# Kernel optimization log

Hardware: AMD Instinct MI355X
Metric: run time of the kernel (lower is better)

## Reference

```python
import jax, jax.numpy as jnp
import numpy as np

N, D, H1, K = 4096, 128, 256, 128


def setup_inputs() -> dict:
    key = jax.random.key(0)
    ks = jax.random.split(key, 8)
    A = jax.random.uniform(ks[3], (D, D), dtype=jnp.float32)
    A = A * (1.0 - jnp.eye(D, dtype=jnp.float32))  # DAG prob mask, no self-loops
    return {
        "x": jax.random.normal(ks[0], (N, D), dtype=jnp.float32),
        "weight": jax.random.normal(ks[1], (D, D), dtype=jnp.float32) * 0.1,
        "bias": jax.random.normal(ks[2], (1, D), dtype=jnp.float32) * 0.1,
        "A": A,
        "W1": jax.random.normal(ks[4], (D, H1), dtype=jnp.float32) * 0.1,
        "b1": jax.random.normal(ks[5], (H1,), dtype=jnp.float32) * 0.1,
        "W2": jax.random.normal(ks[6], (H1, K), dtype=jnp.float32) * 0.1,
        "b2": jax.random.normal(ks[7], (K,), dtype=jnp.float32) * 0.1,
    }


def reference(x, weight, bias, A, W1, b1, W2, b2):
    # to_adj (eval path): masked weights
    W = weight * A                                   # [D, D]
    y = x @ W + bias                                 # [N, D]
    # __expand__ builds diag(y[n]) [N,D,D]; since e[n,i,:] = y[n,i]*I[i,:],
    # the first Linear collapses to a per-row scaling of W1 (same math, fused):
    # e @ W1 -> y[n,i] * W1[i,:]
    h1 = jax.nn.relu(y[:, :, None] * W1[None, :, :] + b1)   # [N, D, H1]
    f = (h1 @ W2 + b2).sum(axis=2)                   # [N, D] (sum over output dim)
    # h_func, method='gnn'
    I = jnp.eye(D, dtype=x.dtype)
    A2 = jnp.square(W)
    M = I + A2 / D
    E = jnp.linalg.matrix_power(M, D - 1)
    h_val = (E.T * M).sum() - D
    # l1_reg (same prob mask in eval)
    reg = jnp.abs(W).sum()
    return (f, h_val, reg)
```

## Files before the change

### kernel.cpp

```cpp
#include <hip/hip_runtime.h>

#define NN 4096
#define DD 128
#define HH1 256

#define WS_S    0
#define WS_S2   16384
#define WS_S3   32768
#define WS_S4   49152
#define WS_W2S  65536
#define WS_B2S  65792
#define WS_TACC 65808
#define WS_DONE 65824
#define WS_REGP 65840

__device__ __forceinline__ float waveReduce(float v) {
#pragma unroll
  for (int off = 32; off > 0; off >>= 1) v += __shfl_down(v, off, 64);
  return v;
}

__global__ __launch_bounds__(256) void kA(
    const float* __restrict__ weight, const float* __restrict__ Amat,
    const float* __restrict__ W2, const float* __restrict__ b2,
    float* __restrict__ ws) {
  const int b = blockIdx.x, tid = threadIdx.x;
  if (b < 64) {
    __shared__ float s_lds[DD * DD];
    const float4* w4 = (const float4*)weight;
    const float4* a4 = (const float4*)Amat;
    float4* s4 = (float4*)s_lds;
    const float inv = 1.0f / 128.0f;
    for (int e = tid; e < DD * DD / 4; e += 256) {
      float4 wv = w4[e], av = a4[e], o;
      float t;
      t = wv.x * av.x; o.x = t * t * inv;
      t = wv.y * av.y; o.y = t * t * inv;
      t = wv.z * av.z; o.z = t * t * inv;
      t = wv.w * av.w; o.w = t * t * inv;
      s4[e] = o;
    }
    __syncthreads();
    const int i = (b << 1) + (tid >> 7), j = tid & 127;
    const float* row = &s_lds[i * DD];
    float acc = 0.f;
#pragma unroll 8
    for (int k = 0; k < DD; ++k) acc = fmaf(row[k], s_lds[k * DD + j], acc);
    ws[WS_S2 + i * DD + j] = acc;
  } else if (b < 72) {
    const int base = (b - 64) * 2048;
    const float inv = 1.0f / 128.0f;
    for (int e = tid; e < 2048; e += 256) {
      const int idx = base + e;
      const float w = weight[idx] * Amat[idx];
      ws[WS_S + idx] = w * w * inv;
    }
  } else if (b == 72) {
    const float4* r = (const float4*)(W2 + tid * 128);
    float4 s4 = make_float4(0.f, 0.f, 0.f, 0.f);
#pragma unroll 8
    for (int k = 0; k < 32; ++k) {
      const float4 v = r[k];
      s4.x += v.x; s4.y += v.y; s4.z += v.z; s4.w += v.w;
    }
    ws[WS_W2S + tid] = (s4.x + s4.y) + (s4.z + s4.w);
  } else if (b == 73) {
    __shared__ float red[4];
    float v = (tid < 128) ? b2[tid] : 0.f;
    v = waveReduce(v);
    if ((tid & 63) == 0) red[tid >> 6] = v;
    __syncthreads();
    if (tid == 0) ws[WS_B2S] = (red[0] + red[1]) + (red[2] + red[3]);
    if (tid >= 64 && tid < 74) ws[WS_TACC + (tid - 64)] = 0.f;
    if (tid == 96) *(unsigned int*)(ws + WS_DONE) = 0u;
  } else {
    const int bb = b - 74;
    const int base = bb * 2048;
    float s = 0.f;
    for (int e = tid; e < 2048; e += 256) {
      const int idx = base + e;
      s += fabsf(weight[idx] * Amat[idx]);
    }
    s = waveReduce(s);
    __shared__ float red[4];
    if ((tid & 63) == 0) red[tid >> 6] = s;
    __syncthreads();
    if (tid == 0) ws[WS_REGP + bb] = (red[0] + red[1]) + (red[2] + red[3]);
  }
}

__global__ __launch_bounds__(256) void kB(
    const float* __restrict__ x, const float* __restrict__ weight,
    const float* __restrict__ Amat, const float* __restrict__ bias,
    const float* __restrict__ W1, const float* __restrict__ b1v,
    float* __restrict__ ws, float* __restrict__ out) {
  const int tid = threadIdx.x;
  if (blockIdx.x < 128) {
    const int sb = blockIdx.x;
    const bool isS4 = sb >= 64;
    const int mb = isS4 ? sb - 64 : sb;
    const float* __restrict__ L = ws + WS_S2;
    const float* __restrict__ R = ws + (isS4 ? WS_S2 : WS_S);
    float* __restrict__ O = ws + (isS4 ? WS_S4 : WS_S3);
    const int i = (mb << 1) + (tid >> 7), j = tid & 127;
    float acc = 0.f;
#pragma unroll 8
    for (int k = 0; k < DD; ++k) acc = fmaf(L[i * DD + k], R[k * DD + j], acc);
    O[i * DD + j] = acc;
    return;
  }
  __shared__ float xs[64 * 132];
  __shared__ float4 fq[4 * 256];
  __shared__ float wcol[4 * 128];
  __shared__ float ts[64 * 5];
  const int fb = blockIdx.x - 128;
  const int i0 = (fb & 31) << 2, n0 = (fb >> 5) << 6;
  const float4* x4 = (const float4*)x;
  for (int e = tid; e < 64 * 32; e += 256) {
    const int r = e >> 5, c = e & 31;
    *(float4*)&xs[r * 132 + (c << 2)] = x4[(n0 + r) * 32 + c];
  }
  for (int e = tid; e < 512; e += 256) {
    const int w = e >> 7, k = e & 127;
    const int gi = k * DD + i0 + w;
    wcol[(w << 7) + k] = weight[gi] * Amat[gi];
  }
  const float* w2s = ws + WS_W2S;
  for (int e = tid; e < 1024; e += 256) {
    const int w = e >> 8, j = e & 255;
    fq[(w << 8) + j] = make_float4(W1[(i0 + w) * HH1 + j], b1v[j], w2s[j], 0.f);
  }
  __syncthreads();
  const int w = tid >> 6, l = tid & 63;
  float t = bias[i0 + w];
  const float4* xr = (const float4*)&xs[l * 132];
  const float4* wc = (const float4*)&wcol[w << 7];
#pragma unroll
  for (int k = 0; k < 32; ++k) {
    const float4 xv = xr[k], wv = wc[k];
    t = fmaf(xv.x, wv.x, t);
    t = fmaf(xv.y, wv.y, t);
    t = fmaf(xv.z, wv.z, t);
    t = fmaf(xv.w, wv.w, t);
  }
  float acc = ws[WS_B2S];
  const float4* fp = &fq[w << 8];
#pragma unroll 8
  for (int j = 0; j < HH1; ++j) {
    const float4 c = fp[j];
    acc = fmaf(fmaxf(fmaf(t, c.x, c.y), 0.f), c.z, acc);
  }
  ts[l * 5 + w] = acc;
  __syncthreads();
  if (tid < 64) {
    const float4 o = make_float4(ts[tid * 5 + 0], ts[tid * 5 + 1],
                                 ts[tid * 5 + 2], ts[tid * 5 + 3]);
    *(float4*)&out[(n0 + tid) * DD + i0] = o;
  }
}

__global__ __launch_bounds__(256) void kC(float* __restrict__ ws,
                                          float* __restrict__ out) {
  const int tid = threadIdx.x;
  const int i = (blockIdx.x << 1) + (tid >> 7), j = tid & 127;
  const float* S1 = ws + WS_S;
  const float* S2 = ws + WS_S2;
  const float* S3 = ws + WS_S3;
  const float* S4 = ws + WS_S4;
  const float a2 = S2[i * DD + j], a3 = S3[i * DD + j];
  const float a1 = S1[i * DD + j];
  const float b1t = S1[j * DD + i], b2t = S2[j * DD + i],
              b3t = S3[j * DD + i], b4t = S4[j * DD + i];
  float e7 = 0.f;
#pragma unroll 8
  for (int k = 0; k < DD; ++k) e7 = fmaf(S3[i * DD + k], S4[k * DD + j], e7);
  float c[10];
  c[0] = a1 * b1t;
  c[1] = a2 * b1t;
  c[2] = a2 * b2t;
  c[3] = a3 * b2t;
  c[4] = a3 * b3t;
  c[5] = a3 * b4t;
  c[6] = e7 * b1t;
  c[7] = e7 * b2t;
  c[8] = e7 * b3t;
  c[9] = e7 * b4t;
  __shared__ float red[4][10];
#pragma unroll
  for (int m = 0; m < 10; ++m) {
    const float v = waveReduce(c[m]);
    if ((tid & 63) == 0) red[tid >> 6][m] = v;
  }
  __syncthreads();
  if (tid == 0) {
    float* tacc = ws + WS_TACC;
    for (int m = 0; m < 10; ++m)
      atomicAdd(&tacc[m], (red[0][m] + red[1][m]) + (red[2][m] + red[3][m]));
    __threadfence();
    unsigned int* done = (unsigned int*)(ws + WS_DONE);
    const unsigned int old = atomicAdd(done, 1u);
    if (old == 63u) {
      __threadfence();
      double h = 0.0, C = 8128.0;
      for (int kk = 2; kk <= 11; ++kk) {
        const float tv = atomicAdd(&tacc[kk - 2], 0.0f);
        h += C * (double)tv;
        C = C * (double)(128 - kk) / (double)(kk + 1);
      }
      float reg = 0.f;
      for (int m = 0; m < 8; ++m) reg += ws[WS_REGP + m];
      out[NN * DD] = (float)h;
      out[NN * DD + 1] = reg;
    }
  }
}

extern "C" void kernel_launch(void* const* d_in, const int* in_sizes, int n_in,
                              void* d_out, int out_size, void* d_ws,
                              size_t ws_size, hipStream_t stream) {
  const float* x      = (const float*)d_in[0];
  const float* weight = (const float*)d_in[1];
  const float* bias   = (const float*)d_in[2];
  const float* Amat   = (const float*)d_in[3];
  const float* W1     = (const float*)d_in[4];
  const float* b1v    = (const float*)d_in[5];
  const float* W2     = (const float*)d_in[6];
  const float* b2     = (const float*)d_in[7];
  float* out = (float*)d_out;
  float* ws  = (float*)d_ws;

  kA<<<82, 256, 0, stream>>>(weight, Amat, W2, b2, ws);
  kB<<<128 + 2048, 256, 0, stream>>>(x, weight, Amat, bias, W1, b1v, ws, out);
  kC<<<64, 256, 0, stream>>>(ws, out);
}
```

Measured before the change: 133.4 us.

## Split y=xW into separate transposed GEMM stage and restructure f computation

Adds a pass that transposes x into workspace, computes y^T = (xW+bias)^T in its own kernel with 8 outputs per thread, and then evaluates the ReLU-MLP sum with each thread handling 4 rows while W1 is read as a wave-uniform scalar row. The aim is to stop recomputing the x·W dot product and reloading x tiles inside every one of the 2048 f-blocks, and to raise reuse per loaded W1/b1/W2-sum value. The cost is extra global round trips for x^T and y^T, about 4 MB of workspace, and a fallback to the old path when the workspace is too small. The old three kernels are kept as that fallback.

After: 107.5 us, median of 2. 1.24x faster.

```diff
diff --git a/kernel.cpp b/kernel.cpp
--- a/kernel.cpp
+++ b/kernel.cpp
@@ -8,11 +8,27 @@
 #define WS_S2   16384
 #define WS_S3   32768
 #define WS_S4   49152
-#define WS_W2S  65536
-#define WS_B2S  65792
-#define WS_TACC 65808
-#define WS_DONE 65824
-#define WS_REGP 65840
+#define WS_W    65536
+#define WS_W2S  81920
+#define WS_PAIR 82176
+#define WS_B2S  82688
+#define WS_TACC 82696
+#define WS_DONE 82708
+#define WS_REGP 82712
+#define WS_XT   82944
+#define WS_YT   607232
+#define WS_REQ_FLOATS 1131520
+#define WS_REQ_BYTES  (WS_REQ_FLOATS * 4UL)
+
+#define O_S    0
+#define O_S2   16384
+#define O_S3   32768
+#define O_S4   49152
+#define O_W2S  65536
+#define O_B2S  65792
+#define O_TACC 65808
+#define O_DONE 65824
+#define O_REGP 65840
 
 __device__ __forceinline__ float waveReduce(float v) {
 #pragma unroll
@@ -20,13 +36,16 @@
   return v;
 }
 
-__global__ __launch_bounds__(256) void kA(
+
+__global__ __launch_bounds__(256) void kA2(
     const float* __restrict__ weight, const float* __restrict__ Amat,
     const float* __restrict__ W2, const float* __restrict__ b2,
+    const float* __restrict__ b1v, const float* __restrict__ x,
     float* __restrict__ ws) {
   const int b = blockIdx.x, tid = threadIdx.x;
+  __shared__ float s_lds[DD * DD];
+  __shared__ float xs[128 * 133];
   if (b < 64) {
-    __shared__ float s_lds[DD * DD];
     const float4* w4 = (const float4*)weight;
     const float4* a4 = (const float4*)Amat;
     float4* s4 = (float4*)s_lds;
@@ -53,6 +72,7 @@
     for (int e = tid; e < 2048; e += 256) {
       const int idx = base + e;
       const float w = weight[idx] * Amat[idx];
+      ws[WS_W + idx] = w;
       ws[WS_S + idx] = w * w * inv;
     }
   } else if (b == 72) {
@@ -63,7 +83,9 @@
       const float4 v = r[k];
       s4.x += v.x; s4.y += v.y; s4.z += v.z; s4.w += v.w;
     }
-    ws[WS_W2S + tid] = (s4.x + s4.y) + (s4.z + s4.w);
+    const float w2sv = (s4.x + s4.y) + (s4.z + s4.w);
+    ws[WS_W2S + tid] = w2sv;
+    ((float2*)(ws + WS_PAIR))[tid] = make_float2(b1v[tid], w2sv);
   } else if (b == 73) {
     __shared__ float red[4];
     float v = (tid < 128) ? b2[tid] : 0.f;
@@ -73,7 +95,7 @@
     if (tid == 0) ws[WS_B2S] = (red[0] + red[1]) + (red[2] + red[3]);
     if (tid >= 64 && tid < 74) ws[WS_TACC + (tid - 64)] = 0.f;
     if (tid == 96) *(unsigned int*)(ws + WS_DONE) = 0u;
-  } else {
+  } else if (b < 82) {
     const int bb = b - 74;
     const int base = bb * 2048;
     float s = 0.f;
@@ -82,18 +104,37 @@
       s += fabsf(weight[idx] * Amat[idx]);
     }
     s = waveReduce(s);
-    __shared__ float red[4];
-    if ((tid & 63) == 0) red[tid >> 6] = s;
-    __syncthreads();
-    if (tid == 0) ws[WS_REGP + bb] = (red[0] + red[1]) + (red[2] + red[3]);
-  }
-}
-
-__global__ __launch_bounds__(256) void kB(
-    const float* __restrict__ x, const float* __restrict__ weight,
-    const float* __restrict__ Amat, const float* __restrict__ bias,
-    const float* __restrict__ W1, const float* __restrict__ b1v,
-    float* __restrict__ ws, float* __restrict__ out) {
+    __shared__ float red2[4];
+    if ((tid & 63) == 0) red2[tid >> 6] = s;
+    __syncthreads();
+    if (tid == 0) ws[WS_REGP + bb] = (red2[0] + red2[1]) + (red2[2] + red2[3]);
+  } else {
+    const int n0 = (b - 82) * 128;
+    const float4* x4 = (const float4*)x;
+    for (int e = tid; e < 4096; e += 256) {
+      const int r = e >> 5, c = e & 31;
+      const float4 v = x4[(n0 + r) * 32 + c];
+      float* p = &xs[r * 133 + (c << 2)];
+      p[0] = v.x; p[1] = v.y; p[2] = v.z; p[3] = v.w;
+    }
+    __syncthreads();
+    float* xT = ws + WS_XT;
+    const int c = tid & 31, ks = tid >> 5;
+#pragma unroll 4
+    for (int m = 0; m < 16; ++m) {
+      const int k = ks + (m << 3);
+      float4 o;
+      o.x = xs[((c << 2) + 0) * 133 + k];
+      o.y = xs[((c << 2) + 1) * 133 + k];
+      o.z = xs[((c << 2) + 2) * 133 + k];
+      o.w = xs[((c << 2) + 3) * 133 + k];
+      *(float4*)&xT[k * NN + n0 + (c << 2)] = o;
+    }
+  }
+}
+
+__global__ __launch_bounds__(256) void kB2(const float* __restrict__ bias,
+                                           float* __restrict__ ws) {
   const int tid = threadIdx.x;
   if (blockIdx.x < 128) {
     const int sb = blockIdx.x;
@@ -109,82 +150,83 @@
     O[i * DD + j] = acc;
     return;
   }
-  __shared__ float xs[64 * 132];
-  __shared__ float4 fq[4 * 256];
-  __shared__ float wcol[4 * 128];
-  __shared__ float ts[64 * 5];
-  const int fb = blockIdx.x - 128;
-  const int i0 = (fb & 31) << 2, n0 = (fb >> 5) << 6;
-  const float4* x4 = (const float4*)x;
-  for (int e = tid; e < 64 * 32; e += 256) {
-    const int r = e >> 5, c = e & 31;
-    *(float4*)&xs[r * 132 + (c << 2)] = x4[(n0 + r) * 32 + c];
-  }
-  for (int e = tid; e < 512; e += 256) {
-    const int w = e >> 7, k = e & 127;
-    const int gi = k * DD + i0 + w;
-    wcol[(w << 7) + k] = weight[gi] * Amat[gi];
-  }
-  const float* w2s = ws + WS_W2S;
-  for (int e = tid; e < 1024; e += 256) {
-    const int w = e >> 8, j = e & 255;
-    fq[(w << 8) + j] = make_float4(W1[(i0 + w) * HH1 + j], b1v[j], w2s[j], 0.f);
-  }
-  __syncthreads();
-  const int w = tid >> 6, l = tid & 63;
-  float t = bias[i0 + w];
-  const float4* xr = (const float4*)&xs[l * 132];
-  const float4* wc = (const float4*)&wcol[w << 7];
-#pragma unroll
-  for (int k = 0; k < 32; ++k) {
-    const float4 xv = xr[k], wv = wc[k];
-    t = fmaf(xv.x, wv.x, t);
-    t = fmaf(xv.y, wv.y, t);
-    t = fmaf(xv.z, wv.z, t);
-    t = fmaf(xv.w, wv.w, t);
-  }
-  float acc = ws[WS_B2S];
-  const float4* fp = &fq[w << 8];
-#pragma unroll 8
-  for (int j = 0; j < HH1; ++j) {
-    const float4 c = fp[j];
-    acc = fmaf(fmaxf(fmaf(t, c.x, c.y), 0.f), c.z, acc);
-  }
-  ts[l * 5 + w] = acc;
-  __syncthreads();
-  if (tid < 64) {
-    const float4 o = make_float4(ts[tid * 5 + 0], ts[tid * 5 + 1],
-                                 ts[tid * 5 + 2], ts[tid * 5 + 3]);
-    *(float4*)&out[(n0 + tid) * DD + i0] = o;
-  }
-}
-
-__global__ __launch_bounds__(256) void kC(float* __restrict__ ws,
-                                          float* __restrict__ out) {
+  const int kb = blockIdx.x - 128;
+  const int n0 = (kb & 15) << 8, i0 = (kb >> 4) << 3;
+  const int n = n0 + tid;
+  const float* __restrict__ xT = ws + WS_XT;
+  const float* __restrict__ Wm = ws + WS_W;
+  float* __restrict__ yT = ws + WS_YT;
+  float acc[8];
+#pragma unroll
+  for (int q = 0; q < 8; ++q) acc[q] = 0.f;
+#pragma unroll 8
+  for (int k = 0; k < DD; ++k) {
+    const float xv = xT[k * NN + n];
+    const float* Wk = Wm + k * DD + i0;
+#pragma unroll
+    for (int q = 0; q < 8; ++q) acc[q] = fmaf(Wk[q], xv, acc[q]);
+  }
+#pragma unroll
+  for (int q = 0; q < 8; ++q) yT[(i0 + q) * NN + n] = acc[q] + bias[i0 + q];
+}
+
+__global__ __launch_bounds__(256) void kC2(const float* __restrict__ W1,
+                                           float* __restrict__ ws,
+                                           float* __restrict__ out) {
   const int tid = threadIdx.x;
-  const int i = (blockIdx.x << 1) + (tid >> 7), j = tid & 127;
+  if (blockIdx.x < 512) {
+    __shared__ float ts[256 * 5];
+    const int fb = blockIdx.x;
+    const int n0 = (fb >> 5) << 8, i0 = (fb & 31) << 2;
+    const int w = tid >> 6, l = tid & 63;
+    const int iu = __builtin_amdgcn_readfirstlane(i0 + w);
+    const float* __restrict__ yT = ws + WS_YT;
+    float t[4];
+#pragma unroll
+    for (int q = 0; q < 4; ++q) t[q] = yT[iu * NN + n0 + (q << 6) + l];
+    const float sb2 = ws[WS_B2S];
+    float acc[4];
+#pragma unroll
+    for (int q = 0; q < 4; ++q) acc[q] = sb2;
+    const float* __restrict__ W1row = W1 + iu * HH1;
+    const float2* __restrict__ pr = (const float2*)(ws + WS_PAIR);
+#pragma unroll 8
+    for (int j = 0; j < HH1; ++j) {
+      const float sw1 = W1row[j];
+      const float2 p = pr[j];
+      const float vb = p.x;
+#pragma unroll
+      for (int q = 0; q < 4; ++q) {
+        const float h = fmaxf(fmaf(t[q], sw1, vb), 0.f);
+        acc[q] = fmaf(h, p.y, acc[q]);
+      }
+    }
+#pragma unroll
+    for (int q = 0; q < 4; ++q) ts[((q << 6) + l) * 5 + w] = acc[q];
+    __syncthreads();
+    const int m = tid;
+    float4 o;
+    o.x = ts[m * 5 + 0]; o.y = ts[m * 5 + 1];
+    o.z = ts[m * 5 + 2]; o.w = ts[m * 5 + 3];
+    *(float4*)&out[(n0 + m) * DD + i0] = o;
+    return;
+  }
+  const int tb = blockIdx.x - 512;
+  const int i = (tb << 1) + (tid >> 7), j = tid & 127;
   const float* S1 = ws + WS_S;
   const float* S2 = ws + WS_S2;
   const float* S3 = ws + WS_S3;
   const float* S4 = ws + WS_S4;
-  const float a2 = S2[i * DD + j], a3 = S3[i * DD + j];
-  const float a1 = S1[i * DD + j];
+  const float a1 = S1[i * DD + j], a2 = S2[i * DD + j], a3 = S3[i * DD + j];
   const float b1t = S1[j * DD + i], b2t = S2[j * DD + i],
               b3t = S3[j * DD + i], b4t = S4[j * DD + i];
   float e7 = 0.f;
 #pragma unroll 8
   for (int k = 0; k < DD; ++k) e7 = fmaf(S3[i * DD + k], S4[k * DD + j], e7);
   float c[10];
-  c[0] = a1 * b1t;
-  c[1] = a2 * b1t;
-  c[2] = a2 * b2t;
-  c[3] = a3 * b2t;
-  c[4] = a3 * b3t;
-  c[5] = a3 * b4t;
-  c[6] = e7 * b1t;
-  c[7] = e7 * b2t;
-  c[8] = e7 * b3t;
-  c[9] = e7 * b4t;
+  c[0] = a1 * b1t; c[1] = a2 * b1t; c[2] = a2 * b2t; c[3] = a3 * b2t;
+  c[4] = a3 * b3t; c[5] = a3 * b4t; c[6] = e7 * b1t; c[7] = e7 * b2t;
+  c[8] = e7 * b3t; c[9] = e7 * b4t;
   __shared__ float red[4][10];
 #pragma unroll
   for (int m = 0; m < 10; ++m) {
@@ -215,6 +257,193 @@
   }
 }
 
+__global__ __launch_bounds__(256) void kA_old(
+    const float* __restrict__ weight, const float* __restrict__ Amat,
+    const float* __restrict__ W2, const float* __restrict__ b2,
+    float* __restrict__ ws) {
+  const int b = blockIdx.x, tid = threadIdx.x;
+  if (b < 64) {
+    __shared__ float s_lds[DD * DD];
+    const float4* w4 = (const float4*)weight;
+    const float4* a4 = (const float4*)Amat;
+    float4* s4 = (float4*)s_lds;
+    const float inv = 1.0f / 128.0f;
+    for (int e = tid; e < DD * DD / 4; e += 256) {
+      float4 wv = w4[e], av = a4[e], o;
+      float t;
+      t = wv.x * av.x; o.x = t * t * inv;
+      t = wv.y * av.y; o.y = t * t * inv;
+      t = wv.z * av.z; o.z = t * t * inv;
+      t = wv.w * av.w; o.w = t * t * inv;
+      s4[e] = o;
+    }
+    __syncthreads();
+    const int i = (b << 1) + (tid >> 7), j = tid & 127;
+    const float* row = &s_lds[i * DD];
+    float acc = 0.f;
+#pragma unroll 8
+    for (int k = 0; k < DD; ++k) acc = fmaf(row[k], s_lds[k * DD + j], acc);
+    ws[O_S2 + i * DD + j] = acc;
+  } else if (b < 72) {
+    const int base = (b - 64) * 2048;
+    const float inv = 1.0f / 128.0f;
+    for (int e = tid; e < 2048; e += 256) {
+      const int idx = base + e;
+      const float w = weight[idx] * Amat[idx];
+      ws[O_S + idx] = w * w * inv;
+    }
+  } else if (b == 72) {
+    const float4* r = (const float4*)(W2 + tid * 128);
+    float4 s4 = make_float4(0.f, 0.f, 0.f, 0.f);
+#pragma unroll 8
+    for (int k = 0; k < 32; ++k) {
+      const float4 v = r[k];
+      s4.x += v.x; s4.y += v.y; s4.z += v.z; s4.w += v.w;
+    }
+    ws[O_W2S + tid] = (s4.x + s4.y) + (s4.z + s4.w);
+  } else if (b == 73) {
+    __shared__ float red[4];
+    float v = (tid < 128) ? b2[tid] : 0.f;
+    v = waveReduce(v);
+    if ((tid & 63) == 0) red[tid >> 6] = v;
+    __syncthreads();
+    if (tid == 0) ws[O_B2S] = (red[0] + red[1]) + (red[2] + red[3]);
+    if (tid >= 64 && tid < 74) ws[O_TACC + (tid - 64)] = 0.f;
+    if (tid == 96) *(unsigned int*)(ws + O_DONE) = 0u;
+  } else {
+    const int bb = b - 74;
+    const int base = bb * 2048;
+    float s = 0.f;
+    for (int e = tid; e < 2048; e += 256) {
+      const int idx = base + e;
+      s += fabsf(weight[idx] * Amat[idx]);
+    }
+    s = waveReduce(s);
+    __shared__ float red[4];
+    if ((tid & 63) == 0) red[tid >> 6] = s;
+    __syncthreads();
+    if (tid == 0) ws[O_REGP + bb] = (red[0] + red[1]) + (red[2] + red[3]);
+  }
+}
+
+__global__ __launch_bounds__(256) void kB_old(
+    const float* __restrict__ x, const float* __restrict__ weight,
+    const float* __restrict__ Amat, const float* __restrict__ bias,
+    const float* __restrict__ W1, const float* __restrict__ b1v,
+    float* __restrict__ ws, float* __restrict__ out) {
+  const int tid = threadIdx.x;
+  if (blockIdx.x < 128) {
+    const int sb = blockIdx.x;
+    const bool isS4 = sb >= 64;
+    const int mb = isS4 ? sb - 64 : sb;
+    const float* __restrict__ L = ws + O_S2;
+    const float* __restrict__ R = ws + (isS4 ? O_S2 : O_S);
+    float* __restrict__ O = ws + (isS4 ? O_S4 : O_S3);
+    const int i = (mb << 1) + (tid >> 7), j = tid & 127;
+    float acc = 0.f;
+#pragma unroll 8
+    for (int k = 0; k < DD; ++k) acc = fmaf(L[i * DD + k], R[k * DD + j], acc);
+    O[i * DD + j] = acc;
+    return;
+  }
+  __shared__ float xs[64 * 132];
+  __shared__ float4 fq[4 * 256];
+  __shared__ float wcol[4 * 128];
+  __shared__ float ts[64 * 5];
+  const int fb = blockIdx.x - 128;
+  const int i0 = (fb & 31) << 2, n0 = (fb >> 5) << 6;
+  const float4* x4 = (const float4*)x;
+  for (int e = tid; e < 64 * 32; e += 256) {
+    const int r = e >> 5, c = e & 31;
+    *(float4*)&xs[r * 132 + (c << 2)] = x4[(n0 + r) * 32 + c];
+  }
+  for (int e = tid; e < 512; e += 256) {
+    const int w = e >> 7, k = e & 127;
+    const int gi = k * DD + i0 + w;
+    wcol[(w << 7) + k] = weight[gi] * Amat[gi];
+  }
+  const float* w2s = ws + O_W2S;
+  for (int e = tid; e < 1024; e += 256) {
+    const int w = e >> 8, j = e & 255;
+    fq[(w << 8) + j] = make_float4(W1[(i0 + w) * HH1 + j], b1v[j], w2s[j], 0.f);
+  }
+  __syncthreads();
+  const int w = tid >> 6, l = tid & 63;
+  float t = bias[i0 + w];
+  const float4* xr = (const float4*)&xs[l * 132];
+  const float4* wc = (const float4*)&wcol[w << 7];
+#pragma unroll
+  for (int k = 0; k < 32; ++k) {
+    const float4 xv = xr[k], wv = wc[k];
+    t = fmaf(xv.x, wv.x, t);
+    t = fmaf(xv.y, wv.y, t);
+    t = fmaf(xv.z, wv.z, t);
+    t = fmaf(xv.w, wv.w, t);
+  }
+  float acc = ws[O_B2S];
+  const float4* fp = &fq[w << 8];
+#pragma unroll 8
+  for (int j = 0; j < HH1; ++j) {
+    const float4 c = fp[j];
+    acc = fmaf(fmaxf(fmaf(t, c.x, c.y), 0.f), c.z, acc);
+  }
+  ts[l * 5 + w] = acc;
+  __syncthreads();
+  if (tid < 64) {
+    const float4 o = make_float4(ts[tid * 5 + 0], ts[tid * 5 + 1],
+                                 ts[tid * 5 + 2], ts[tid * 5 + 3]);
+    *(float4*)&out[(n0 + tid) * DD + i0] = o;
+  }
+}
+
+__global__ __launch_bounds__(256) void kC_old(float* __restrict__ ws,
+                                              float* __restrict__ out) {
+  const int tid = threadIdx.x;
+  const int i = (blockIdx.x << 1) + (tid >> 7), j = tid & 127;
+  const float* S1 = ws + O_S;
+  const float* S2 = ws + O_S2;
+  const float* S3 = ws + O_S3;
+  const float* S4 = ws + O_S4;
+  const float a1 = S1[i * DD + j], a2 = S2[i * DD + j], a3 = S3[i * DD + j];
+  const float b1t = S1[j * DD + i], b2t = S2[j * DD + i],
+              b3t = S3[j * DD + i], b4t = S4[j * DD + i];
+  float e7 = 0.f;
+#pragma unroll 8
+  for (int k = 0; k < DD; ++k) e7 = fmaf(S3[i * DD + k], S4[k * DD + j], e7);
+  float c[10];
+  c[0] = a1 * b1t; c[1] = a2 * b1t; c[2] = a2 * b2t; c[3] = a3 * b2t;
+  c[4] = a3 * b3t; c[5] = a3 * b4t; c[6] = e7 * b1t; c[7] = e7 * b2t;
+  c[8] = e7 * b3t; c[9] = e7 * b4t;
+  __shared__ float red[4][10];
+#pragma unroll
+  for (int m = 0; m < 10; ++m) {
+    const float v = waveReduce(c[m]);
+    if ((tid & 63) == 0) red[tid >> 6][m] = v;
+  }
+  __syncthreads();
+  if (tid == 0) {
+    float* tacc = ws + O_TACC;
+    for (int m = 0; m < 10; ++m)
+      atomicAdd(&tacc[m], (red[0][m] + red[1][m]) + (red[2][m] + red[3][m]));
+    __threadfence();
+    unsigned int* done = (unsigned int*)(ws + O_DONE);
+    const unsigned int old = atomicAdd(done, 1u);
+    if (old == 63u) {
+      __threadfence();
+      double h = 0.0, C = 8128.0;
+      for (int kk = 2; kk <= 11; ++kk) {
+        const float tv = atomicAdd(&tacc[kk - 2], 0.0f);
+        h += C * (double)tv;
+        C = C * (double)(128 - kk) / (double)(kk + 1);
+      }
+      float reg = 0.f;
+      for (int m = 0; m < 8; ++m) reg += ws[O_REGP + m];
+      out[NN * DD] = (float)h;
+      out[NN * DD + 1] = reg;
+    }
+  }
+}
+
 extern "C" void kernel_launch(void* const* d_in, const int* in_sizes, int n_in,
                               void* d_out, int out_size, void* d_ws,
                               size_t ws_size, hipStream_t stream) {
@@ -229,7 +458,14 @@
   float* out = (float*)d_out;
   float* ws  = (float*)d_ws;
 
-  kA<<<82, 256, 0, stream>>>(weight, Amat, W2, b2, ws);
-  kB<<<128 + 2048, 256, 0, stream>>>(x, weight, Amat, bias, W1, b1v, ws, out);
-  kC<<<64, 256, 0, stream>>>(ws, out);
-}
+  if (ws_size >= WS_REQ_BYTES) {
+    kA2<<<114, 256, 0, stream>>>(weight, Amat, W2, b2, b1v, x, ws);
+    kB2<<<384, 256, 0, stream>>>(bias, ws);
+    kC2<<<576, 256, 0, stream>>>(W1, ws, out);
+  } else {
+    kA_old<<<82, 256, 0, stream>>>(weight, Amat, W2, b2, ws);
+    kB_old<<<128 + 2048, 256, 0, stream>>>(x, weight, Amat, bias, W1, b1v, ws,
+                                           out);
+    kC_old<<<64, 256, 0, stream>>>(ws, out);
+  }
+}
```
